# Optimization experiments

Hardware: AMD Instinct MI355X
Metric: run time of the kernel (lower is better)

Reference implementation:

```python
import jax, jax.numpy as jnp
import numpy as np

K_PERIODS = 6


def setup_inputs() -> dict:
    key = jax.random.key(0)
    x = jax.random.normal(key, (16, 2048, 128), dtype=jnp.float32)
    return {"x": x}


def reference(x):
    # x: [B, T, N] -> out: [B, K, Pmax, N].
    # Pmax is data-dependent in the torch original (max selected period); here we
    # use the static upper bound Pmax = T so shapes are jit-static. Columns
    # p >= P_row are zero, matching the original's zero padding.
    B, T, N = x.shape
    BN = B * N
    seqs = jnp.transpose(x, (0, 2, 1)).reshape(BN, T)  # [BN, T]

    # --- top-k nonzero frequencies by spectral energy ---
    spec = jnp.fft.rfft(seqs, axis=-1)
    mag2 = spec.real ** 2 + spec.imag ** 2
    mag2 = mag2.at[:, 0].set(0.0)  # kill DC bin
    k = min(K_PERIODS, mag2.shape[-1] - 1)
    _, kidx = jax.lax.top_k(mag2, k)          # [BN, K]
    kidx = jnp.maximum(kidx, 1)

    # --- per-(row, freq) period geometry ---
    P = jnp.maximum(T // kidx, 1)             # [BN, K] period length
    cycles = jnp.maximum(T // P, 1)           # [BN, K] number of full cycles
    take = cycles * P
    base = jnp.maximum(T - take, 0)           # [BN, K] start offset

    # --- fold-and-average via scatter-add (no [BN,K,Cmax,Pmax] blowup) ---
    # element at time t >= base maps to phase p = (t - base) % P, averaged over cycles
    t = jnp.arange(T, dtype=jnp.int32)
    rel = t[None, None, :] - base[:, :, None]          # [BN, K, T]
    valid = rel >= 0
    p = jnp.where(valid, rel % P[:, :, None], 0)       # phase index in [0, P)
    vals = jnp.where(valid, seqs[:, None, :], 0.0)     # [BN, K, T]

    row = jnp.arange(BN * k, dtype=jnp.int32).reshape(BN, k, 1)
    seg_ids = row * T + p                               # flat segment id
    sums = jax.ops.segment_sum(vals.reshape(-1), seg_ids.reshape(-1),
                               num_segments=BN * k * T)
    seg = sums.reshape(BN, k, T) / cycles[:, :, None].astype(vals.dtype)

    out = seg.reshape(B, N, k, T).transpose(0, 2, 3, 1)  # [B, K, Pmax=T, N]
    return out
```

## Files before the change

kernel.cpp:

```cpp
#include <hip/hip_runtime.h>
#include <stdint.h>

#define TB   256
#define FT   512
#define TLEN 2048
#define NB   16
#define NCH  128
#define BN   (NB*NCH)
#define KP   6

typedef unsigned long long u64;

__device__ inline float2 cmul(float2 a, float2 b) {
  return make_float2(a.x * b.x - a.y * b.y, a.x * b.y + a.y * b.x);
}
__device__ inline float2 cadd(float2 a, float2 b) { return make_float2(a.x + b.x, a.y + b.y); }
__device__ inline float2 csub(float2 a, float2 b) { return make_float2(a.x - b.x, a.y - b.y); }
__device__ inline float2 cmni(float2 a) { return make_float2(a.y, -a.x); }

#define PAD(o) ((o) + ((o) >> 4))

__global__ __launch_bounds__(256) void k_prep(const float* __restrict__ x,
                                              float* __restrict__ seqs,
                                              float4* __restrict__ out4, int n4) {
  int bid = blockIdx.x;
  if (bid < 1024) {
    __shared__ float tile[64][65];
    int tb = bid & 31, nb = (bid >> 5) & 1, b = bid >> 6;
    int t0 = tb * 64, n0 = nb * 64;
    int tx = threadIdx.x & 63, ty = threadIdx.x >> 6;
#pragma unroll
    for (int tt = ty; tt < 64; tt += 4)
      tile[tt][tx] = x[(size_t)(b * TLEN + t0 + tt) * NCH + n0 + tx];
    __syncthreads();
#pragma unroll
    for (int nn = ty; nn < 64; nn += 4)
      seqs[(size_t)(b * NCH + n0 + nn) * TLEN + t0 + tx] = tile[tx][nn];
  } else {
    int i = (bid - 1024) * 256 + threadIdx.x;
    if (i < n4) out4[i] = make_float4(0.f, 0.f, 0.f, 0.f);
  }
}

__global__ __launch_bounds__(FT, 8) void k_fft_fold(const float* __restrict__ seqs,
                                                    float* __restrict__ out) {
  __shared__ __align__(16) float2 bufA[2176];
  __shared__ __align__(16) float2 bufB[2176];
  __shared__ float2 tw[512];
  __shared__ u64 wmax[8];
  __shared__ int4 prm[2][KP];
  int tid = threadIdx.x, lane = tid & 63, wv = tid >> 6;
  int r0 = blockIdx.x * 2;
  const float* row0 = seqs + (size_t)r0 * TLEN;

#pragma unroll
  for (int kk = 0; kk < 4; kk++) {
    int t = tid + kk * FT;
    bufA[PAD(t)] = make_float2(row0[t], row0[t + TLEN]);
  }
  {
    float sn, cs;
    sincosf((-6.283185307179586f / 2048.f) * (float)tid, &sn, &cs);
    tw[tid & 511] = make_float2(cs, sn);
  }

  float2* xb = bufA;
  float2* yb = bufB;
#pragma unroll
  for (int st2 = 0; st2 < 10; st2 += 2) {
    int s = 1 << st2;
    __syncthreads();
    int i = tid;
    int q = i & (s - 1);
    int cb = i - q;
    float2 A0 = xb[PAD(i)];
    float2 A1 = xb[PAD(i + 512)];
    float2 A2 = xb[PAD(i + 1024)];
    float2 A3 = xb[PAD(i + 1536)];
    float2 S02 = cadd(A0, A2), D02 = csub(A0, A2);
    float2 S13 = cadd(A1, A3), D13 = csub(A1, A3);
    float2 b0 = cadd(S02, S13);
    float2 b1 = cadd(D02, cmni(D13));
    float2 b2 = csub(S02, S13);
    float2 b3 = csub(D02, cmni(D13));
    float2 w1 = tw[cb];
    float2 w2 = cmul(w1, w1);
    float2 w3 = cmul(w1, w2);
    int o = q + 4 * cb;
    yb[PAD(o)]         = b0;
    yb[PAD(o + s)]     = cmul(w1, b1);
    yb[PAD(o + 2 * s)] = cmul(w2, b2);
    yb[PAD(o + 3 * s)] = cmul(w3, b3);
    float2* t2 = xb; xb = yb; yb = t2;
  }
  __syncthreads();
#pragma unroll
  for (int ii = 0; ii < 2; ii++) {
    int i = tid + ii * FT;
    float2 a = bufB[PAD(i)];
    float2 b = bufB[PAD(i + 1024)];
    bufA[PAD(i)]        = cadd(a, b);
    bufA[PAD(i + 1024)] = csub(a, b);
  }
  __syncthreads();

  u64 kra[2], krb[2];
#pragma unroll
  for (int ii = 0; ii < 2; ii++) {
    int i = tid + ii * FT;
    int kb = i + 1;
    float2 zk = bufA[PAD(kb)];
    float2 zc = bufA[PAD(2048 - kb)];
    float ax = zk.x + zc.x, ay = zk.y - zc.y;
    float bx = zk.x - zc.x, by = zk.y + zc.y;
    float m2a = ax * ax + ay * ay;
    float m2b = bx * bx + by * by;
    kra[ii] = ((u64)__float_as_uint(m2a) << 32) | (unsigned)(0xFFFFFFFFu - (unsigned)kb);
    krb[ii] = ((u64)__float_as_uint(m2b) << 32) | (unsigned)(0xFFFFFFFFu - (unsigned)kb);
  }
  __syncthreads();
  u64* keys = (u64*)bufA;
#pragma unroll
  for (int ii = 0; ii < 2; ii++) {
    int i = tid + ii * FT;
    keys[i] = kra[ii];
    keys[1024 + i] = krb[ii];
  }
  {
    const float4* s4 = (const float4*)row0;
    float4* r4 = (float4*)bufB;
#pragma unroll
    for (int ii = 0; ii < 2; ii++) r4[tid + ii * FT] = s4[tid + ii * FT];
  }
  __syncthreads();

  int rw2 = wv >> 2;
  u64* kb2 = keys + rw2 * 1024;
  int t2 = tid & 255;
  for (int r = 0; r < KP; r++) {
    u64 best = 0ull;
#pragma unroll
    for (int j = 0; j < 4; j++) {
      u64 v = kb2[t2 + j * 256];
      best = v > best ? v : best;
    }
    for (int off = 32; off > 0; off >>= 1) {
      u64 o = __shfl_down(best, off);
      best = o > best ? o : best;
    }
    if (lane == 0) wmax[wv] = best;
    __syncthreads();
    if (t2 == 0) {
      best = wmax[rw2 * 4];
#pragma unroll
      for (int w = 1; w < 4; w++) {
        u64 v = wmax[rw2 * 4 + w];
        best = v > best ? v : best;
      }
      int bin = (int)(0xFFFFFFFFu - (unsigned)(best & 0xFFFFFFFFull));
      if (bin < 1 || bin > 1024) bin = 1;
      kb2[bin - 1] = 0ull;
      int P = TLEN / bin;
      int cyc = TLEN / P;
      int base = TLEN - cyc * P;
      prm[rw2][r] = make_int4(P, base, cyc, 0);
    }
    __syncthreads();
  }

  float* srows = (float*)bufB;
  for (int task = wv; task < 2 * KP; task += 8) {
    int rw = task & 1, k = task >> 1;
    int4 pr = prm[rw][k];
    int P = pr.x, base = pr.y, cyc = pr.z;
    float inv = 1.0f / (float)cyc;
    const float* srow = srows + rw * TLEN;
    int row = r0 + rw, b = row >> 7, n = row & 127;
    float* dst = out + (size_t)(b * KP + k) * TLEN * NCH + n;

    if (P >= 64) {
      for (int p = lane; p < P; p += 64) {
        const float* sp = srow + base + p;
        float s = 0.f;
        for (int c = 0; c < cyc; c++) s += sp[c * P];
        dst[(size_t)p * NCH] = s * inv;
      }
    } else {
      int wc = 64 / P, u = wc * P, ci = lane / P;
      float v = 0.f;
      if (lane < u) {
        for (int c0 = 0; c0 < cyc; c0 += wc) {
          int c = c0 + ci;
          if (c < cyc) v += srow[base + c0 * P + lane];
        }
      }
      for (int s = P; s < u; s <<= 1) {
        float o = __shfl_down(v, s);
        if (lane + s < u) v += o;
      }
      if (lane < P) dst[(size_t)lane * NCH] = v * inv;
    }
  }
}

extern "C" void kernel_launch(void* const* d_in, const int* in_sizes, int n_in,
                              void* d_out, int out_size, void* d_ws, size_t ws_size,
                              hipStream_t stream) {
  const float* x = (const float*)d_in[0];
  float* out = (float*)d_out;
  float* seqs = (float*)d_ws;

  int n4 = out_size / 4;
  int fill_blocks = (n4 + 255) / 256;
  k_prep<<<1024 + fill_blocks, 256, 0, stream>>>(x, seqs, (float4*)out, n4);
  k_fft_fold<<<BN / 2, FT, 0, stream>>>(seqs, out);
}
```

Baseline: 146.0 us.

## Replace shared-memory top-k rounds with per-wave shuffle top-k and paired float2 stores

Top-k selection now runs per wavefront on register keys with xor-shuffle max reductions, producing 6 candidates per wave. A single wave then merges the 48 candidates, which removes the 12 block-wide barriers and shared key buffer of the old loop. The fold stage assigns one wave per period index and writes both rows of the block together as float2 stores, so global writes are coalesced pairs instead of strided scalars. Ties between equal 64-bit keys cannot occur because bin indices are unique. Rows whose period is shorter than the max must now write explicit zeros up to Pm.

```diff
diff --git a/kernel.cpp b/kernel.cpp
--- a/kernel.cpp
+++ b/kernel.cpp
@@ -42,12 +42,39 @@
   }
 }
 
+__device__ inline float foldval(const float* __restrict__ srow, int P, int base,
+                                int cyc, int p0, int lane) {
+  if (P >= 64) {
+    int p = p0 + lane;
+    if (p >= P) return 0.f;
+    const float* sp = srow + base + p;
+    float s = 0.f;
+    for (int c = 0; c < cyc; c++) s += sp[c * P];
+    return s;
+  } else {
+    if (p0 > 0) return 0.f;
+    int wc = 64 / P, u = wc * P, ci = lane / P;
+    float v = 0.f;
+    if (lane < u) {
+      for (int c0 = 0; c0 < cyc; c0 += wc) {
+        int c = c0 + ci;
+        if (c < cyc) v += srow[base + c0 * P + lane];
+      }
+    }
+    for (int s = P; s < u; s <<= 1) {
+      float o = __shfl_down(v, s);
+      if (lane + s < u) v += o;
+    }
+    return (lane < P) ? v : 0.f;
+  }
+}
+
 __global__ __launch_bounds__(FT, 8) void k_fft_fold(const float* __restrict__ seqs,
                                                     float* __restrict__ out) {
   __shared__ __align__(16) float2 bufA[2176];
   __shared__ __align__(16) float2 bufB[2176];
   __shared__ float2 tw[512];
-  __shared__ u64 wmax[8];
+  __shared__ u64 cand[2][8][KP];
   __shared__ int4 prm[2][KP];
   int tid = threadIdx.x, lane = tid & 63, wv = tid >> 6;
   int r0 = blockIdx.x * 2;
@@ -118,87 +145,74 @@
     kra[ii] = ((u64)__float_as_uint(m2a) << 32) | (unsigned)(0xFFFFFFFFu - (unsigned)kb);
     krb[ii] = ((u64)__float_as_uint(m2b) << 32) | (unsigned)(0xFFFFFFFFu - (unsigned)kb);
   }
-  __syncthreads();
-  u64* keys = (u64*)bufA;
-#pragma unroll
-  for (int ii = 0; ii < 2; ii++) {
-    int i = tid + ii * FT;
-    keys[i] = kra[ii];
-    keys[1024 + i] = krb[ii];
-  }
   {
     const float4* s4 = (const float4*)row0;
     float4* r4 = (float4*)bufB;
 #pragma unroll
     for (int ii = 0; ii < 2; ii++) r4[tid + ii * FT] = s4[tid + ii * FT];
   }
-  __syncthreads();
-
-  int rw2 = wv >> 2;
-  u64* kb2 = keys + rw2 * 1024;
-  int t2 = tid & 255;
-  for (int r = 0; r < KP; r++) {
-    u64 best = 0ull;
-#pragma unroll
-    for (int j = 0; j < 4; j++) {
-      u64 v = kb2[t2 + j * 256];
-      best = v > best ? v : best;
-    }
-    for (int off = 32; off > 0; off >>= 1) {
-      u64 o = __shfl_down(best, off);
-      best = o > best ? o : best;
-    }
-    if (lane == 0) wmax[wv] = best;
-    __syncthreads();
-    if (t2 == 0) {
-      best = wmax[rw2 * 4];
-#pragma unroll
-      for (int w = 1; w < 4; w++) {
-        u64 v = wmax[rw2 * 4 + w];
-        best = v > best ? v : best;
-      }
-      int bin = (int)(0xFFFFFFFFu - (unsigned)(best & 0xFFFFFFFFull));
-      if (bin < 1 || bin > 1024) bin = 1;
-      kb2[bin - 1] = 0ull;
-      int P = TLEN / bin;
-      int cyc = TLEN / P;
-      int base = TLEN - cyc * P;
-      prm[rw2][r] = make_int4(P, base, cyc, 0);
-    }
-    __syncthreads();
-  }
-
-  float* srows = (float*)bufB;
-  for (int task = wv; task < 2 * KP; task += 8) {
-    int rw = task & 1, k = task >> 1;
-    int4 pr = prm[rw][k];
-    int P = pr.x, base = pr.y, cyc = pr.z;
-    float inv = 1.0f / (float)cyc;
-    const float* srow = srows + rw * TLEN;
-    int row = r0 + rw, b = row >> 7, n = row & 127;
-    float* dst = out + (size_t)(b * KP + k) * TLEN * NCH + n;
-
-    if (P >= 64) {
-      for (int p = lane; p < P; p += 64) {
-        const float* sp = srow + base + p;
-        float s = 0.f;
-        for (int c = 0; c < cyc; c++) s += sp[c * P];
-        dst[(size_t)p * NCH] = s * inv;
-      }
-    } else {
-      int wc = 64 / P, u = wc * P, ci = lane / P;
-      float v = 0.f;
-      if (lane < u) {
-        for (int c0 = 0; c0 < cyc; c0 += wc) {
-          int c = c0 + ci;
-          if (c < cyc) v += srow[base + c0 * P + lane];
-        }
-      }
-      for (int s = P; s < u; s <<= 1) {
-        float o = __shfl_down(v, s);
-        if (lane + s < u) v += o;
-      }
-      if (lane < P) dst[(size_t)lane * NCH] = v * inv;
+
+#pragma unroll
+  for (int rw = 0; rw < 2; rw++) {
+    u64 l0 = rw ? krb[0] : kra[0];
+    u64 l1 = rw ? krb[1] : kra[1];
+#pragma unroll 1
+    for (int r = 0; r < KP; r++) {
+      u64 m = l0 > l1 ? l0 : l1;
+#pragma unroll
+      for (int off = 1; off < 64; off <<= 1) {
+        u64 o = __shfl_xor(m, off);
+        m = o > m ? o : m;
+      }
+      if (l0 == m) l0 = 0ull;
+      if (l1 == m) l1 = 0ull;
+      if (lane == 0) cand[rw][wv][r] = m;
+    }
+  }
+  __syncthreads();
+
+  if (wv == 0 || wv == 4) {
+    int rw = wv >> 2;
+    u64 c = (lane < 48) ? cand[rw][lane / KP][lane % KP] : 0ull;
+#pragma unroll 1
+    for (int r = 0; r < KP; r++) {
+      u64 m = c;
+#pragma unroll
+      for (int off = 1; off < 64; off <<= 1) {
+        u64 o = __shfl_xor(m, off);
+        m = o > m ? o : m;
+      }
+      if (c == m) c = 0ull;
+      if (lane == 0) {
+        int bin = (int)(0xFFFFFFFFu - (unsigned)(m & 0xFFFFFFFFull));
+        if (bin < 1 || bin > 1024) bin = 1;
+        int P = TLEN / bin;
+        int cyc = TLEN / P;
+        int base = TLEN - cyc * P;
+        prm[rw][r] = make_int4(P, base, cyc, 0);
+      }
+    }
+  }
+  __syncthreads();
+
+  const float* srow0 = (const float*)bufB;
+  const float* srow1 = srow0 + TLEN;
+  if (wv < KP) {
+    int k = wv;
+    int4 p0v = prm[0][k];
+    int4 p1v = prm[1][k];
+    int P0 = p0v.x, base0 = p0v.y, cyc0 = p0v.z;
+    int P1 = p1v.x, base1 = p1v.y, cyc1 = p1v.z;
+    float inv0 = 1.0f / (float)cyc0, inv1 = 1.0f / (float)cyc1;
+    int Pm = P0 > P1 ? P0 : P1;
+    int b = r0 >> 7, n0 = r0 & 127;
+    float2* dst2 = (float2*)(out + (size_t)(b * KP + k) * TLEN * NCH + n0);
+    for (int pc = 0; pc < Pm; pc += 64) {
+      float v0 = foldval(srow0, P0, base0, cyc0, pc, lane);
+      float v1 = foldval(srow1, P1, base1, cyc1, pc, lane);
+      int p = pc + lane;
+      if (p < Pm)
+        dst2[(size_t)p * (NCH / 2)] = make_float2(v0 * inv0, v1 * inv1);
     }
   }
 }
```

Result: slower. 154.5 us (+5.9%).
